# Kernel optimization log

Hardware: AMD Instinct MI355X
Metric: run time of the kernel (lower is better)

The kernel has to match this reference:

```python
import jax, jax.numpy as jnp
import numpy as np

EPS = 1e-5

def _ln(x, g, b):
    mu = jnp.mean(x, axis=-1, keepdims=True)
    var = jnp.mean(jnp.square(x - mu), axis=-1, keepdims=True)
    return (x - mu) * jax.lax.rsqrt(var + EPS) * g + b

def setup_inputs() -> dict:
    B, T, D, E, H, M = 2, 2048, 1024, 8, 512, 2048
    key = jax.random.key(0)
    ks = jax.random.split(key, 24)
    s = 0.02
    inp = {}
    inp['x'] = jax.random.normal(ks[0], (B, T, D), jnp.float32)
    flat = jnp.arange(M, dtype=jnp.int32) * 2  # unique token ids over B*T
    inp['index_b'] = flat // T
    inp['index_t'] = flat % T
    # shared SwiGLU (hidden = H)
    inp['sw1'] = jax.random.normal(ks[1], (H, D), jnp.float32) * s
    inp['sb1'] = jnp.zeros((H,), jnp.float32)
    inp['sw2'] = jax.random.normal(ks[2], (H, D), jnp.float32) * s
    inp['sb2'] = jnp.zeros((H,), jnp.float32)
    inp['sw3'] = jax.random.normal(ks[3], (D, H), jnp.float32) * s
    inp['sb3'] = jnp.zeros((D,), jnp.float32)
    inp['s_ln_g'] = jnp.ones((H,), jnp.float32)
    inp['s_ln_b'] = jnp.zeros((H,), jnp.float32)
    # gates
    inp['sg_w'] = jax.random.normal(ks[4], (1, D), jnp.float32) * s
    inp['sg_b'] = jnp.zeros((1,), jnp.float32)
    inp['eg_w'] = jax.random.normal(ks[5], (E, D), jnp.float32) * s
    inp['eg_b'] = jnp.zeros((E,), jnp.float32)
    inp['exp_bias'] = jnp.zeros((E,), jnp.float32)
    # per-expert SwiGLU stacks
    inp['ew1'] = jax.random.normal(ks[6], (E, H, D), jnp.float32) * s
    inp['eb1'] = jnp.zeros((E, H), jnp.float32)
    inp['ew2'] = jax.random.normal(ks[7], (E, H, D), jnp.float32) * s
    inp['eb2'] = jnp.zeros((E, H), jnp.float32)
    inp['ew3'] = jax.random.normal(ks[8], (E, D, H), jnp.float32) * s
    inp['eb3'] = jnp.zeros((E, D), jnp.float32)
    inp['sel_ln_g'] = jnp.ones((H,), jnp.float32)
    inp['sel_ln_b'] = jnp.zeros((H,), jnp.float32)
    return inp

def _forward(x, index_b, index_t, sw1, sb1, sw2, sb2, sw3, sb3, s_ln_g, s_ln_b,
             sg_w, sg_b, eg_w, eg_b, exp_bias, ew1, eb1, ew2, eb2, ew3, eb3,
             sel_ln_g, sel_ln_b):
    # shared SwiGLU over all tokens: [B,T,D]
    x1 = jnp.einsum('btd,hd->bth', x, sw1) + sb1
    x2 = jnp.einsum('btd,hd->bth', x, sw2) + sb2
    sh = _ln(jax.nn.silu(x1) * x2, s_ln_g, s_ln_b)
    shared_out = jnp.einsum('bth,dh->btd', sh, sw3) + sb3
    # MoE tokens
    x_moe = x[index_b, index_t]  # [M,D]
    shared_scores = jax.nn.sigmoid(x_moe @ sg_w.T + sg_b)       # [M,1]
    expert_scores = jax.nn.sigmoid(x_moe @ eg_w.T + eg_b)       # [M,E]
    top1_idx = jnp.argmax(expert_scores + exp_bias, axis=-1)    # [M]
    top1_score = jnp.take_along_axis(expert_scores, top1_idx[:, None], axis=-1)  # [M,1]
    weights = jax.nn.softmax(jnp.concatenate([shared_scores, top1_score], axis=-1), axis=-1)
    shared_w, expert_w = weights[:, 0], weights[:, 1]
    shared_moe_out = shared_out[index_b, index_t] * shared_w[:, None]
    # per-expert SwiGLU computed densely for all E, then token selects its expert
    h1 = jnp.einsum('md,ehd->meh', x_moe, ew1) + eb1  # [M,E,H]
    h2 = jnp.einsum('md,ehd->meh', x_moe, ew2) + eb2
    z = _ln(jax.nn.silu(h1) * h2, sel_ln_g, sel_ln_b)
    out_all = jnp.einsum('meh,edh->med', z, ew3) + eb3  # [M,E,D]
    expert_out = jnp.take_along_axis(out_all, top1_idx[:, None, None], axis=1)[:, 0]  # [M,D]
    expert_moe_out = expert_out * expert_w[:, None]
    final_out = shared_out.at[index_b, index_t].set(shared_moe_out + expert_moe_out)
    return final_out

def reference(x, index_b, index_t, sw1, sb1, sw2, sb2, sw3, sb3, s_ln_g, s_ln_b,
              sg_w, sg_b, eg_w, eg_b, exp_bias, ew1, eb1, ew2, eb2, ew3, eb3,
              sel_ln_g, sel_ln_b):
    return _forward(x, index_b, index_t, sw1, sb1, sw2, sb2, sw3, sb3, s_ln_g, s_ln_b,
                    sg_w, sg_b, eg_w, eg_b, exp_bias, ew1, eb1, ew2, eb2, ew3, eb3,
                    sel_ln_g, sel_ln_b)
```

## Files before the change

kernel.cpp:

```cpp
#include <hip/hip_runtime.h>
#include <cstdint>

typedef unsigned short u16;
typedef __bf16 bf16x8 __attribute__((ext_vector_type(8)));
typedef float f32x4 __attribute__((ext_vector_type(4)));

#define T_SEQ  2048
#define D_DIM  1024
#define H_DIM  512
#define E_NUM  8
#define M_TOK  2048
#define BT_TOK 4096
#define MAXP   3072
#define NSPLIT_NONE (1 << 28)

static __device__ __forceinline__ u16 f2bf(float f) {
    union { float f; uint32_t u; } v; v.f = f;
    uint32_t u = v.u;
    return (u16)((u + 0x7FFFu + ((u >> 16) & 1u)) >> 16);
}
static __device__ __forceinline__ uint32_t pack2(float a, float b) {
    return (uint32_t)f2bf(a) | ((uint32_t)f2bf(b) << 16);
}

static __device__ __forceinline__ void gl_lds16(const u16* g, u16* l) {
    __builtin_amdgcn_global_load_lds(
        (const __attribute__((address_space(1))) uint32_t*)g,
        (__attribute__((address_space(3))) uint32_t*)l, 16, 0, 0);
}

static __device__ __forceinline__ int find_expert(int m, const int* __restrict__ base) {
    int e = 0;
    #pragma unroll
    for (int ee = 0; ee < E_NUM - 1; ++ee)
        if (m >= base[ee + 1]) e = ee + 1;
    return e;
}

static __device__ __forceinline__ void cvt4(const float* __restrict__ s,
                                            u16* __restrict__ d, long off) {
    float4 v = ((const float4*)s)[off];
    uint2 o;
    o.x = pack2(v.x, v.y);
    o.y = pack2(v.z, v.w);
    ((uint2*)d)[off] = o;
}


__device__ __forceinline__ void gating_body(
    int m,
    const float* __restrict__ x,
    const int* __restrict__ ib, const int* __restrict__ itx,
    const float* __restrict__ sgw, const float* __restrict__ sgb,
    const float* __restrict__ egw, const float* __restrict__ egb,
    const float* __restrict__ ebias,
    float* __restrict__ shw, float* __restrict__ expw,
    int* __restrict__ top1, int* __restrict__ rowidx,
    float* xs, float* sc)
{
    int tid = threadIdx.x;
    int row = ib[m] * T_SEQ + itx[m];
    if (tid == 0) rowidx[m] = row;
    const float* xr = x + (size_t)row * D_DIM;
    ((float4*)xs)[tid] = ((const float4*)xr)[tid];
    __syncthreads();
    int lane = tid & 63, w4 = tid >> 6;
    for (int sidx = w4; sidx < 9; sidx += 4) {
        const float* wr = (sidx == 0) ? sgw : (egw + (size_t)(sidx - 1) * D_DIM);
        float acc = 0.f;
        #pragma unroll
        for (int i = 0; i < 4; ++i) {
            int idx = i * 64 + lane;
            float4 xv = ((const float4*)xs)[idx];
            float4 wv = ((const float4*)wr)[idx];
            acc += xv.x * wv.x + xv.y * wv.y + xv.z * wv.z + xv.w * wv.w;
        }
        #pragma unroll
        for (int o = 32; o > 0; o >>= 1) acc += __shfl_xor(acc, o);
        if (lane == 0) sc[sidx] = acc;
    }
    __syncthreads();
    if (tid == 0) {
        float ss = 1.f / (1.f + expf(-(sc[0] + sgb[0])));
        float es[E_NUM];
        float best = -1e30f; int bi = 0;
        #pragma unroll
        for (int e = 0; e < E_NUM; ++e) {
            es[e] = 1.f / (1.f + expf(-(sc[1 + e] + egb[e])));
            float t = es[e] + ebias[e];
            if (t > best) { best = t; bi = e; }
        }
        float ts = es[bi];
        shw[m]  = 1.f / (1.f + expf(ts - ss));
        expw[m] = 1.f / (1.f + expf(ss - ts));
        top1[m] = bi;
    }
}

__device__ __forceinline__ void bucket_body(
    const int* __restrict__ top1,
    int* __restrict__ base, int* __restrict__ cnt, int* __restrict__ perm,
    int* sm)
{
    int* lc  = sm;
    int* lb  = sm + E_NUM;
    int* cur = sm + 2 * E_NUM + 1;
    int tid = threadIdx.x;
    if (tid < E_NUM) { lc[tid] = 0; cur[tid] = 0; }
    __syncthreads();
    for (int m = tid; m < M_TOK; m += 256) atomicAdd(&lc[top1[m]], 1);
    __syncthreads();
    if (tid == 0) {
        int bacc = 0;
        for (int e = 0; e < E_NUM; ++e) { lb[e] = bacc; bacc += (lc[e] + 127) & ~127; }
        lb[E_NUM] = bacc;
    }
    __syncthreads();
    for (int m = tid; m < M_TOK; m += 256) {
        int e = top1[m];
        int pos = lb[e] + atomicAdd(&cur[e], 1);
        perm[pos] = m;
    }
    if (tid <= E_NUM) base[tid] = lb[tid];
    if (tid < E_NUM)  cnt[tid]  = lc[tid];
}

template<bool SEL>
__device__ __forceinline__ void ln_body(
    int m,
    const float* __restrict__ X,
    const float* __restrict__ g, const float* __restrict__ b,
    u16* __restrict__ out,
    const int* __restrict__ base, const int* __restrict__ cnt,
    float* red)
{
    int tid = threadIdx.x;
    if (SEL) {
        bool valid = false;
        int tot = base[E_NUM];
        if (m < tot) {
            int e = find_expert(m, base);
            valid = (m - base[e]) < cnt[e];
        }
        if (!valid) {
            out[(size_t)m * H_DIM + tid] = 0;
            out[(size_t)m * H_DIM + tid + 256] = 0;
            return;
        }
    }
    const float* row = X + (size_t)m * D_DIM;
    float a0 = row[tid],       c0 = row[H_DIM + tid];
    float a1 = row[tid + 256], c1 = row[H_DIM + tid + 256];
    float v0 = (a0 / (1.f + expf(-a0))) * c0;
    float v1 = (a1 / (1.f + expf(-a1))) * c1;
    float s = v0 + v1, s2 = v0 * v0 + v1 * v1;
    #pragma unroll
    for (int o = 32; o > 0; o >>= 1) {
        s  += __shfl_xor(s, o);
        s2 += __shfl_xor(s2, o);
    }
    int w = tid >> 6;
    if ((tid & 63) == 0) { red[w] = s; red[4 + w] = s2; }
    __syncthreads();
    s  = red[0] + red[1] + red[2] + red[3];
    s2 = red[4] + red[5] + red[6] + red[7];
    float mu  = s * (1.f / H_DIM);
    float var = s2 * (1.f / H_DIM) - mu * mu;
    float inv = rsqrtf(var + 1e-5f);
    out[(size_t)m * H_DIM + tid]       = f2bf((v0 - mu) * inv * g[tid] + b[tid]);
    out[(size_t)m * H_DIM + tid + 256] = f2bf((v1 - mu) * inv * g[tid + 256] + b[tid + 256]);
}

template<int MODE, int KLEN>
__device__ __forceinline__ void gemm_body(
    int bn, int bm,
    const u16* __restrict__ A, int lda,
    const u16* __restrict__ W0, const u16* __restrict__ W1, int nsplit,
    const float* __restrict__ b0, const float* __restrict__ b1,
    float* __restrict__ C,
    const int* __restrict__ base, const int* __restrict__ cnt,
    const int* __restrict__ perm, const int* __restrict__ rowidx,
    const float* __restrict__ shw, const float* __restrict__ expw,
    u16* lds)
{
    constexpr int NITER = KLEN / 64;
    const int tid   = threadIdx.x;
    const int mbase = bm * 128;

    int pend = 0;
    if (MODE >= 2) {
        const int tot = base[E_NUM];
        if (mbase >= tot) return;
        int e = find_expert(mbase, base);
        pend = base[e] + cnt[e];
        if (mbase >= pend) return;
        const size_t wstride = (size_t)H_DIM * D_DIM;
        W0 += (size_t)e * wstride;
        if (MODE == 2) W1 += (size_t)e * wstride;
        b0 += e * ((MODE == 2) ? H_DIM : D_DIM);
        if (MODE == 2) b1 += e * H_DIM;
    }

    const int w  = tid >> 6;
    const int l  = tid & 63;
    const int sr = tid >> 3;
    const int sc = tid & 7;

    const u16* agp[4];
    #pragma unroll
    for (int t = 0; t < 4; ++t) {
        int r = t * 32 + sr;
        int grow;
        if (MODE == 2) {
            int p  = mbase + r;
            int pp = (p < pend) ? p : (pend - 1);
            grow = rowidx[perm[pp]];
        } else {
            grow = mbase + r;
        }
        agp[t] = A + (size_t)grow * lda + (sc ^ (r & 7)) * 8;
    }
    const u16* bgp[4];
    #pragma unroll
    for (int t = 0; t < 4; ++t) {
        int r = t * 32 + sr;
        int n = bn * 128 + r;
        bgp[t] = ((n < nsplit) ? (W0 + (size_t)n * KLEN)
                               : (W1 + (size_t)(n - nsplit) * KLEN)) + (sc ^ (r & 7)) * 8;
    }

    const int l16 = l & 15, quad = l >> 4;
    const int wm = w >> 1, wn = w & 1;

    int avo[4], bvo[4];
    #pragma unroll
    for (int i = 0; i < 4; ++i) {
        int R = wm * 64 + i * 16 + l16;
        avo[i] = R * 128 + ((quad ^ (R & 7)) * 16);
    }
    #pragma unroll
    for (int j = 0; j < 4; ++j) {
        int R = wn * 64 + j * 16 + l16;
        bvo[j] = 16384 + R * 128 + ((quad ^ (R & 7)) * 16);
    }

    f32x4 acc[4][4];
    #pragma unroll
    for (int i = 0; i < 4; ++i)
        #pragma unroll
        for (int j = 0; j < 4; ++j)
            acc[i][j] = (f32x4){0.f, 0.f, 0.f, 0.f};

    const int kstart = (bm + bn * 3) & (NITER - 1);
    const char* ldsc = (const char*)lds;

    {
        int k0 = kstart * 64;
        #pragma unroll
        for (int t = 0; t < 4; ++t)
            gl_lds16(agp[t] + k0, lds + t * 2048 + w * 512);
        #pragma unroll
        for (int t = 0; t < 4; ++t)
            gl_lds16(bgp[t] + k0, lds + 8192 + t * 2048 + w * 512);
    }
    __syncthreads();

    for (int it = 0; it < NITER; ++it) {
        const int cur = it & 1;
        if (it + 1 < NITER) {
            int k0 = ((it + 1 + kstart) & (NITER - 1)) * 64;
            u16* lb = lds + (cur ^ 1) * 16384;
            #pragma unroll
            for (int t = 0; t < 4; ++t)
                gl_lds16(agp[t] + k0, lb + t * 2048 + w * 512);
            #pragma unroll
            for (int t = 0; t < 4; ++t)
                gl_lds16(bgp[t] + k0, lb + 8192 + t * 2048 + w * 512);
        }
        const char* lb = ldsc + cur * 32768;
        #pragma unroll
        for (int kx = 0; kx < 2; ++kx) {
            bf16x8 av[4], bv[4];
            #pragma unroll
            for (int i = 0; i < 4; ++i)
                av[i] = *(const bf16x8*)(lb + (avo[i] ^ (kx * 64)));
            #pragma unroll
            for (int j = 0; j < 4; ++j)
                bv[j] = *(const bf16x8*)(lb + (bvo[j] ^ (kx * 64)));
            #pragma unroll
            for (int i = 0; i < 4; ++i)
                #pragma unroll
                for (int j = 0; j < 4; ++j)
                    acc[i][j] = __builtin_amdgcn_mfma_f32_16x16x32_bf16(av[i], bv[j], acc[i][j], 0, 0, 0);
        }
        if (it + 1 < NITER) __syncthreads();
    }

    if (MODE == 3) {
        #pragma unroll
        for (int i = 0; i < 4; ++i) {
            #pragma unroll
            for (int rr = 0; rr < 4; ++rr) {
                int p = mbase + wm * 64 + i * 16 + quad * 4 + rr;
                if (p < pend) {
                    int tok = perm[p];
                    int row = rowidx[tok];
                    float sw = shw[tok], ew = expw[tok];
                    float* outr = C + (size_t)row * D_DIM;
                    #pragma unroll
                    for (int j = 0; j < 4; ++j) {
                        int gn = bn * 128 + wn * 64 + j * 16 + l16;
                        outr[gn] = outr[gn] * sw + (acc[i][j][rr] + b0[gn]) * ew;
                    }
                }
            }
        }
    } else {
        #pragma unroll
        for (int i = 0; i < 4; ++i) {
            #pragma unroll
            for (int rr = 0; rr < 4; ++rr) {
                int gm = mbase + wm * 64 + i * 16 + quad * 4 + rr;
                float* outr = C + (size_t)gm * D_DIM;
                #pragma unroll
                for (int j = 0; j < 4; ++j) {
                    int gn = bn * 128 + wn * 64 + j * 16 + l16;
                    float bias = (gn < nsplit) ? b0[gn] : b1[gn - nsplit];
                    outr[gn] = acc[i][j][rr] + bias;
                }
            }
        }
    }
}


__global__ __launch_bounds__(256)
void k_cvt1_gating(const float* __restrict__ x,
                   const float* __restrict__ sw1, const float* __restrict__ sw2,
                   u16* __restrict__ xb, u16* __restrict__ sw1b, u16* __restrict__ sw2b,
                   const int* __restrict__ ib, const int* __restrict__ itx,
                   const float* __restrict__ sgw, const float* __restrict__ sgb,
                   const float* __restrict__ egw, const float* __restrict__ egb,
                   const float* __restrict__ ebias,
                   float* __restrict__ shw, float* __restrict__ expw,
                   int* __restrict__ top1, int* __restrict__ rowidx)
{
    __shared__ __align__(16) float smem[D_DIM + 16];
    int bx = blockIdx.x;
    if (bx >= 5120) {
        gating_body(bx - 5120, x, ib, itx, sgw, sgb, egw, egb, ebias,
                    shw, expw, top1, rowidx, smem, smem + D_DIM);
        return;
    }
    long i = (long)bx * 256 + threadIdx.x;
    if      (i < 1048576) cvt4(x,   xb,   i);
    else if (i < 1179648) cvt4(sw1, sw1b, i - 1048576);
    else                  cvt4(sw2, sw2b, i - 1179648);
}

__global__ __launch_bounds__(256)
void k_g1_bucket_cvt2(const u16* __restrict__ xb,
                      const u16* __restrict__ sw1b, const u16* __restrict__ sw2b,
                      const float* __restrict__ sb1, const float* __restrict__ sb2,
                      float* __restrict__ x12,
                      const int* __restrict__ top1,
                      int* __restrict__ basep, int* __restrict__ cntp, int* __restrict__ perm,
                      const float* __restrict__ sw3, const float* __restrict__ ew1,
                      const float* __restrict__ ew2, const float* __restrict__ ew3,
                      u16* __restrict__ sw3b, u16* __restrict__ ew1b,
                      u16* __restrict__ ew2b, u16* __restrict__ ew3b)
{
    __shared__ __align__(16) u16 lds[2 * (128 + 128) * 64];
    int bx = blockIdx.x;
    if (bx < 256) {
        gemm_body<0, 1024>(bx & 7, bx >> 3, xb, D_DIM, sw1b, sw2b, H_DIM, sb1, sb2, x12,
                           nullptr, nullptr, nullptr, nullptr, nullptr, nullptr, lds);
        return;
    }
    if (bx == 256) {
        bucket_body(top1, basep, cntp, perm, (int*)lds);
        return;
    }
    long i = (long)(bx - 257) * 256 + threadIdx.x;
    if      (i <  131072) cvt4(sw3, sw3b, i);
    else if (i < 1179648) cvt4(ew1, ew1b, i - 131072);
    else if (i < 2228224) cvt4(ew2, ew2b, i - 1179648);
    else                  cvt4(ew3, ew3b, i - 2228224);
}

__global__ __launch_bounds__(256)
void k_ln_e1(const float* __restrict__ x12,
             const float* __restrict__ g, const float* __restrict__ b,
             u16* __restrict__ shn,
             const u16* __restrict__ xb,
             const u16* __restrict__ ew1b, const u16* __restrict__ ew2b,
             const float* __restrict__ eb1, const float* __restrict__ eb2,
             float* __restrict__ h12,
             const int* __restrict__ basep, const int* __restrict__ cntp,
             const int* __restrict__ perm, const int* __restrict__ rowidx)
{
    __shared__ __align__(16) u16 lds[2 * (128 + 128) * 64];
    int bx = blockIdx.x;
    if (bx < BT_TOK) {
        ln_body<false>(bx, x12, g, b, shn, nullptr, nullptr, (float*)lds);
    } else {
        int b2 = bx - BT_TOK;
        gemm_body<2, 1024>(b2 & 7, b2 >> 3, xb, D_DIM, ew1b, ew2b, H_DIM, eb1, eb2, h12,
                           basep, cntp, perm, rowidx, nullptr, nullptr, lds);
    }
}

__global__ __launch_bounds__(256)
void k_g2_lnsel(const u16* __restrict__ shn, const u16* __restrict__ sw3b,
                const float* __restrict__ sb3, float* __restrict__ out,
                const float* __restrict__ h12,
                const float* __restrict__ selg, const float* __restrict__ selb,
                u16* __restrict__ z,
                const int* __restrict__ basep, const int* __restrict__ cntp)
{
    __shared__ __align__(16) u16 lds[2 * (128 + 128) * 64];
    int bx = blockIdx.x;
    if (bx < 256) {
        gemm_body<1, 512>(bx & 7, bx >> 3, shn, H_DIM, sw3b, sw3b, NSPLIT_NONE, sb3, sb3, out,
                          nullptr, nullptr, nullptr, nullptr, nullptr, nullptr, lds);
    } else {
        ln_body<true>(bx - 256, h12, selg, selb, z, basep, cntp, (float*)lds);
    }
}

__global__ __launch_bounds__(256)
void k_e2(const u16* __restrict__ z, const u16* __restrict__ ew3b,
          const float* __restrict__ eb3, float* __restrict__ out,
          const int* __restrict__ basep, const int* __restrict__ cntp,
          const int* __restrict__ perm, const int* __restrict__ rowidx,
          const float* __restrict__ shw, const float* __restrict__ expw)
{
    __shared__ __align__(16) u16 lds[2 * (128 + 128) * 64];
    int bx = blockIdx.x;
    gemm_body<3, 512>(bx & 7, bx >> 3, z, H_DIM, ew3b, ew3b, NSPLIT_NONE, eb3, eb3, out,
                      basep, cntp, perm, rowidx, shw, expw, lds);
}

extern "C" void kernel_launch(void* const* d_in, const int* in_sizes, int n_in,
                              void* d_out, int out_size, void* d_ws, size_t ws_size,
                              hipStream_t stream) {
    const float* x        = (const float*)d_in[0];
    const int*   index_b  = (const int*)d_in[1];
    const int*   index_t  = (const int*)d_in[2];
    const float* sw1      = (const float*)d_in[3];
    const float* sb1      = (const float*)d_in[4];
    const float* sw2      = (const float*)d_in[5];
    const float* sb2      = (const float*)d_in[6];
    const float* sw3      = (const float*)d_in[7];
    const float* sb3      = (const float*)d_in[8];
    const float* s_ln_g   = (const float*)d_in[9];
    const float* s_ln_b   = (const float*)d_in[10];
    const float* sg_w     = (const float*)d_in[11];
    const float* sg_b     = (const float*)d_in[12];
    const float* eg_w     = (const float*)d_in[13];
    const float* eg_b     = (const float*)d_in[14];
    const float* exp_bias = (const float*)d_in[15];
    const float* ew1      = (const float*)d_in[16];
    const float* eb1      = (const float*)d_in[17];
    const float* ew2      = (const float*)d_in[18];
    const float* eb2      = (const float*)d_in[19];
    const float* ew3      = (const float*)d_in[20];
    const float* eb3      = (const float*)d_in[21];
    const float* sel_ln_g = (const float*)d_in[22];
    const float* sel_ln_b = (const float*)d_in[23];
    float* out = (float*)d_out;
    char*  ws  = (char*)d_ws;

    u16*   xb   = (u16*)(ws + 0);
    u16*   sw1b = (u16*)(ws + 8388608);
    u16*   sw2b = (u16*)(ws + 9437184);
    u16*   sw3b = (u16*)(ws + 10485760);
    u16*   ew1b = (u16*)(ws + 11534336);
    u16*   ew2b = (u16*)(ws + 19922944);
    u16*   ew3b = (u16*)(ws + 28311552);
    float* x12  = (float*)(ws + 36700160);
    u16*   sh   = (u16*)(ws + 53477376);
    float* shw    = (float*)(ws + 57671680);
    float* expw   = shw + M_TOK;
    int*   top1   = (int*)(expw + M_TOK);
    int*   rowidx = top1 + M_TOK;
    int*   perm   = rowidx + M_TOK;
    int*   basep  = perm + MAXP;
    int*   cntp   = basep + 16;
    float* h12  = (float*)(ws + 58720256);
    u16*   z    = (u16*)(ws + 71303168);

    k_cvt1_gating<<<dim3(5120 + M_TOK), dim3(256), 0, stream>>>(
        x, sw1, sw2, xb, sw1b, sw2b,
        index_b, index_t, sg_w, sg_b, eg_w, eg_b, exp_bias,
        shw, expw, top1, rowidx);

    k_g1_bucket_cvt2<<<dim3(257 + 12800), dim3(256), 0, stream>>>(
        xb, sw1b, sw2b, sb1, sb2, x12, top1, basep, cntp, perm,
        sw3, ew1, ew2, ew3, sw3b, ew1b, ew2b, ew3b);

    k_ln_e1<<<dim3(BT_TOK + 8 * (MAXP / 128)), dim3(256), 0, stream>>>(
        x12, s_ln_g, s_ln_b, sh,
        xb, ew1b, ew2b, eb1, eb2, h12,
        basep, cntp, perm, rowidx);

    k_g2_lnsel<<<dim3(256 + MAXP), dim3(256), 0, stream>>>(
        sh, sw3b, sb3, out,
        h12, sel_ln_g, sel_ln_b, z, basep, cntp);

    k_e2<<<dim3(8 * (MAXP / 128)), dim3(256), 0, stream>>>(
        z, ew3b, eb3, out, basep, cntp, perm, rowidx, shw, expw);
}
```

Before: 251.9 us.

## Regroup kernel stages so GEMMs co-run and weight conversions overlap with LN

```diff
diff --git a/kernel.cpp b/kernel.cpp
--- a/kernel.cpp
+++ b/kernel.cpp
@@ -37,13 +37,16 @@
     return e;
 }
 
-static __device__ __forceinline__ void cvt4(const float* __restrict__ s,
+static __device__ __forceinline__ void cvt8(const float* __restrict__ s,
                                             u16* __restrict__ d, long off) {
-    float4 v = ((const float4*)s)[off];
-    uint2 o;
-    o.x = pack2(v.x, v.y);
-    o.y = pack2(v.z, v.w);
-    ((uint2*)d)[off] = o;
+    float4 v0 = ((const float4*)s)[off * 2];
+    float4 v1 = ((const float4*)s)[off * 2 + 1];
+    uint4 o;
+    o.x = pack2(v0.x, v0.y);
+    o.y = pack2(v0.z, v0.w);
+    o.z = pack2(v1.x, v1.y);
+    o.w = pack2(v1.z, v1.w);
+    ((uint4*)d)[off] = o;
 }
 
 
@@ -347,51 +350,58 @@
 {
     __shared__ __align__(16) float smem[D_DIM + 16];
     int bx = blockIdx.x;
-    if (bx >= 5120) {
-        gating_body(bx - 5120, x, ib, itx, sgw, sgb, egw, egb, ebias,
+    if (bx >= 2560) {
+        gating_body(bx - 2560, x, ib, itx, sgw, sgb, egw, egb, ebias,
                     shw, expw, top1, rowidx, smem, smem + D_DIM);
         return;
     }
     long i = (long)bx * 256 + threadIdx.x;
-    if      (i < 1048576) cvt4(x,   xb,   i);
-    else if (i < 1179648) cvt4(sw1, sw1b, i - 1048576);
-    else                  cvt4(sw2, sw2b, i - 1179648);
+    if      (i < 524288) cvt8(x,   xb,   i);
+    else if (i < 589824) cvt8(sw1, sw1b, i - 524288);
+    else                 cvt8(sw2, sw2b, i - 589824);
 }
 
 __global__ __launch_bounds__(256)
-void k_g1_bucket_cvt2(const u16* __restrict__ xb,
-                      const u16* __restrict__ sw1b, const u16* __restrict__ sw2b,
-                      const float* __restrict__ sb1, const float* __restrict__ sb2,
-                      float* __restrict__ x12,
-                      const int* __restrict__ top1,
-                      int* __restrict__ basep, int* __restrict__ cntp, int* __restrict__ perm,
-                      const float* __restrict__ sw3, const float* __restrict__ ew1,
-                      const float* __restrict__ ew2, const float* __restrict__ ew3,
-                      u16* __restrict__ sw3b, u16* __restrict__ ew1b,
-                      u16* __restrict__ ew2b, u16* __restrict__ ew3b)
+void k_g1_bucket(const u16* __restrict__ xb,
+                 const u16* __restrict__ sw1b, const u16* __restrict__ sw2b,
+                 const float* __restrict__ sb1, const float* __restrict__ sb2,
+                 float* __restrict__ x12,
+                 const int* __restrict__ top1,
+                 int* __restrict__ basep, int* __restrict__ cntp, int* __restrict__ perm)
 {
     __shared__ __align__(16) u16 lds[2 * (128 + 128) * 64];
     int bx = blockIdx.x;
     if (bx < 256) {
         gemm_body<0, 1024>(bx & 7, bx >> 3, xb, D_DIM, sw1b, sw2b, H_DIM, sb1, sb2, x12,
                            nullptr, nullptr, nullptr, nullptr, nullptr, nullptr, lds);
+    } else {
+        bucket_body(top1, basep, cntp, perm, (int*)lds);
+    }
+}
+
+__global__ __launch_bounds__(256)
+void k_ln_cvt2(const float* __restrict__ x12,
+               const float* __restrict__ g, const float* __restrict__ b,
+               u16* __restrict__ shn,
+               const float* __restrict__ sw3, const float* __restrict__ ew1,
+               const float* __restrict__ ew2,
+               u16* __restrict__ sw3b, u16* __restrict__ ew1b, u16* __restrict__ ew2b)
+{
+    __shared__ __align__(16) float smf[8];
+    int bx = blockIdx.x;
+    if (bx < BT_TOK) {
+        ln_body<false>(bx, x12, g, b, shn, nullptr, nullptr, smf);
         return;
     }
-    if (bx == 256) {
-        bucket_body(top1, basep, cntp, perm, (int*)lds);
-        return;
-    }
-    long i = (long)(bx - 257) * 256 + threadIdx.x;
-    if      (i <  131072) cvt4(sw3, sw3b, i);
-    else if (i < 1179648) cvt4(ew1, ew1b, i - 131072);
-    else if (i < 2228224) cvt4(ew2, ew2b, i - 1179648);
-    else                  cvt4(ew3, ew3b, i - 2228224);
+    long i = (long)(bx - BT_TOK) * 256 + threadIdx.x;
+    if      (i <  65536) cvt8(sw3, sw3b, i);
+    else if (i < 589824) cvt8(ew1, ew1b, i - 65536);
+    else                 cvt8(ew2, ew2b, i - 589824);
 }
 
 __global__ __launch_bounds__(256)
-void k_ln_e1(const float* __restrict__ x12,
-             const float* __restrict__ g, const float* __restrict__ b,
-             u16* __restrict__ shn,
+void k_g2_e1(const u16* __restrict__ shn, const u16* __restrict__ sw3b,
+             const float* __restrict__ sb3, float* __restrict__ out,
              const u16* __restrict__ xb,
              const u16* __restrict__ ew1b, const u16* __restrict__ ew2b,
              const float* __restrict__ eb1, const float* __restrict__ eb2,
@@ -401,31 +411,31 @@
 {
     __shared__ __align__(16) u16 lds[2 * (128 + 128) * 64];
     int bx = blockIdx.x;
-    if (bx < BT_TOK) {
-        ln_body<false>(bx, x12, g, b, shn, nullptr, nullptr, (float*)lds);
-    } else {
-        int b2 = bx - BT_TOK;
-        gemm_body<2, 1024>(b2 & 7, b2 >> 3, xb, D_DIM, ew1b, ew2b, H_DIM, eb1, eb2, h12,
-                           basep, cntp, perm, rowidx, nullptr, nullptr, lds);
-    }
-}
-
-__global__ __launch_bounds__(256)
-void k_g2_lnsel(const u16* __restrict__ shn, const u16* __restrict__ sw3b,
-                const float* __restrict__ sb3, float* __restrict__ out,
-                const float* __restrict__ h12,
-                const float* __restrict__ selg, const float* __restrict__ selb,
-                u16* __restrict__ z,
-                const int* __restrict__ basep, const int* __restrict__ cntp)
-{
-    __shared__ __align__(16) u16 lds[2 * (128 + 128) * 64];
-    int bx = blockIdx.x;
     if (bx < 256) {
         gemm_body<1, 512>(bx & 7, bx >> 3, shn, H_DIM, sw3b, sw3b, NSPLIT_NONE, sb3, sb3, out,
                           nullptr, nullptr, nullptr, nullptr, nullptr, nullptr, lds);
     } else {
-        ln_body<true>(bx - 256, h12, selg, selb, z, basep, cntp, (float*)lds);
-    }
+        int b2 = bx - 256;
+        gemm_body<2, 1024>(b2 & 7, b2 >> 3, xb, D_DIM, ew1b, ew2b, H_DIM, eb1, eb2, h12,
+                           basep, cntp, perm, rowidx, nullptr, nullptr, lds);
+    }
+}
+
+__global__ __launch_bounds__(256)
+void k_lnsel_cvt3(const float* __restrict__ h12,
+                  const float* __restrict__ g, const float* __restrict__ b,
+                  u16* __restrict__ z,
+                  const int* __restrict__ basep, const int* __restrict__ cntp,
+                  const float* __restrict__ ew3, u16* __restrict__ ew3b)
+{
+    __shared__ __align__(16) float smf[8];
+    int bx = blockIdx.x;
+    if (bx < MAXP) {
+        ln_body<true>(bx, h12, g, b, z, basep, cntp, smf);
+        return;
+    }
+    long i = (long)(bx - MAXP) * 256 + threadIdx.x;
+    cvt8(ew3, ew3b, i);
 }
 
 __global__ __launch_bounds__(256)
@@ -490,23 +500,25 @@
     float* h12  = (float*)(ws + 58720256);
     u16*   z    = (u16*)(ws + 71303168);
 
-    k_cvt1_gating<<<dim3(5120 + M_TOK), dim3(256), 0, stream>>>(
+    k_cvt1_gating<<<dim3(2560 + M_TOK), dim3(256), 0, stream>>>(
         x, sw1, sw2, xb, sw1b, sw2b,
         index_b, index_t, sg_w, sg_b, eg_w, eg_b, exp_bias,
         shw, expw, top1, rowidx);
 
-    k_g1_bucket_cvt2<<<dim3(257 + 12800), dim3(256), 0, stream>>>(
-        xb, sw1b, sw2b, sb1, sb2, x12, top1, basep, cntp, perm,
-        sw3, ew1, ew2, ew3, sw3b, ew1b, ew2b, ew3b);
-
-    k_ln_e1<<<dim3(BT_TOK + 8 * (MAXP / 128)), dim3(256), 0, stream>>>(
+    k_g1_bucket<<<dim3(257), dim3(256), 0, stream>>>(
+        xb, sw1b, sw2b, sb1, sb2, x12, top1, basep, cntp, perm);
+
+    k_ln_cvt2<<<dim3(BT_TOK + 4352), dim3(256), 0, stream>>>(
         x12, s_ln_g, s_ln_b, sh,
+        sw3, ew1, ew2, sw3b, ew1b, ew2b);
+
+    k_g2_e1<<<dim3(256 + 8 * (MAXP / 128)), dim3(256), 0, stream>>>(
+        sh, sw3b, sb3, out,
         xb, ew1b, ew2b, eb1, eb2, h12,
         basep, cntp, perm, rowidx);
 
-    k_g2_lnsel<<<dim3(256 + MAXP), dim3(256), 0, stream>>>(
-        sh, sw3b, sb3, out,
-        h12, sel_ln_g, sel_ln_b, z, basep, cntp);
+    k_lnsel_cvt3<<<dim3(MAXP + 2048), dim3(256), 0, stream>>>(
+        h12, sel_ln_g, sel_ln_b, z, basep, cntp, ew3, ew3b);
 
     k_e2<<<dim3(8 * (MAXP / 128)), dim3(256), 0, stream>>>(
         z, ew3b, eb3, out, basep, cntp, perm, rowidx, shw, expw);
```

After: 226.7 us. 1.11x faster.
